# Kernel optimization log

Hardware: AMD Instinct MI355X
Metric: run time of the kernel (lower is better)

Reference implementation:

```python
import jax, jax.numpy as jnp
import numpy as np

BANDWIDTH = 1.0  # init arg `bandwidth`
N, V, C = 8, 2048, 64


def setup_inputs() -> dict:
    key = jax.random.key(0)
    k1, k2 = jax.random.split(key)
    x = jax.random.normal(k1, (N, V, C), dtype=jnp.float32)
    # nn.Parameter(torch.rand(V, V)) -> uniform[0,1)
    weight = jax.random.uniform(k2, (V, V), dtype=jnp.float32)
    return {"x": x, "weight": weight}


def _pairwise_l2(x):
    # x: (N, V, C) -> dist[n,i,j] = ||x[n,i] - x[n,j]||_2, without the O(V^2*C) blow-up
    sq = jnp.sum(x * x, axis=-1)                                  # (N, V)
    d2 = sq[:, :, None] + sq[:, None, :] - 2.0 * jnp.einsum('nic,njc->nij', x, x)
    d2 = jnp.maximum(d2, 0.0)
    # safe sqrt: subgradient 0 at 0 (matches torch.norm), avoids NaN grads on the diagonal
    safe = jnp.where(d2 > 0, d2, 1.0)
    return jnp.where(d2 > 0, jnp.sqrt(safe), 0.0)


def reference(x, weight):
    dist = _pairwise_l2(x)                                        # (N, V, V)
    adj = jnp.exp((-0.5 / (BANDWIDTH ** 2)) * dist)               # Gaussian kernel on L2 (not squared)
    adj = jnp.einsum('nij,jk->nik', adj, weight)                  # (N, V, V) @ (V, V)
    return jax.nn.softmax(adj, axis=-1)
```

## Files before the change

### kernel.cpp

```cpp
#include <hip/hip_runtime.h>
#include <hip/hip_bf16.h>
#include <hip/hip_fp16.h>
#include <math.h>

#define V 2048
#define C 64
#define NB 8
#define M_TOTAL (NB * V)

typedef __attribute__((ext_vector_type(8))) short bf16x8;
typedef __attribute__((ext_vector_type(4))) float f32x4;

static __device__ __forceinline__ unsigned short f2bf(float f) {
    __hip_bfloat16 h = __float2bfloat16(f);
    return *reinterpret_cast<unsigned short*>(&h);
}
static __device__ __forceinline__ unsigned short f2h(float f) {
    __half h = __float2half(f);
    return *reinterpret_cast<unsigned short*>(&h);
}
static __device__ __forceinline__ float h2f(unsigned short u) {
    __half h = *reinterpret_cast<__half*>(&u);
    return __half2float(h);
}

#define GLOAD_LDS16(g, l)                                                        \
    __builtin_amdgcn_global_load_lds((const __attribute__((address_space(1))) void*)(g), \
                                     (__attribute__((address_space(3))) void*)(l), 16, 0, 0)


__global__ __launch_bounds__(256) void adj_mfma(const float* __restrict__ x,
                                                unsigned short* __restrict__ adjb) {
    const int n  = blockIdx.z;
    const int i0 = blockIdx.y * 128;
    const int j0 = blockIdx.x * 128;
    const size_t nV = (size_t)n * V;

    __shared__ short Xi[128][72];
    __shared__ short Xj[128][72];
    __shared__ float Qi[128];
    __shared__ float Qj[128];

    const float* xn = x + nV * C;
    const int tid = threadIdx.x;

    for (int idx = tid; idx < 1024; idx += 256) {
        const int row = idx >> 3;
        const int c8  = (idx & 7) * 8;
        float4 ai0 = *(const float4*)(xn + (size_t)(i0 + row) * C + c8);
        float4 ai1 = *(const float4*)(xn + (size_t)(i0 + row) * C + c8 + 4);
        float4 aj0 = *(const float4*)(xn + (size_t)(j0 + row) * C + c8);
        float4 aj1 = *(const float4*)(xn + (size_t)(j0 + row) * C + c8 + 4);
        bf16x8 pi, pj;
        pi[0] = (short)f2bf(ai0.x); pi[1] = (short)f2bf(ai0.y);
        pi[2] = (short)f2bf(ai0.z); pi[3] = (short)f2bf(ai0.w);
        pi[4] = (short)f2bf(ai1.x); pi[5] = (short)f2bf(ai1.y);
        pi[6] = (short)f2bf(ai1.z); pi[7] = (short)f2bf(ai1.w);
        pj[0] = (short)f2bf(aj0.x); pj[1] = (short)f2bf(aj0.y);
        pj[2] = (short)f2bf(aj0.z); pj[3] = (short)f2bf(aj0.w);
        pj[4] = (short)f2bf(aj1.x); pj[5] = (short)f2bf(aj1.y);
        pj[6] = (short)f2bf(aj1.z); pj[7] = (short)f2bf(aj1.w);
        *(bf16x8*)&Xi[row][c8] = pi;
        *(bf16x8*)&Xj[row][c8] = pj;
    }
    __syncthreads();

    const int wid  = tid >> 6;
    const int lane = tid & 63;
    const int wr = wid >> 1, wc = wid & 1;
    const int lr = lane & 15, lq = lane >> 4;

#pragma unroll
    for (int gg = 0; gg < 2; ++gg) {
        const int g = wid * 2 + gg;
        {
            const short* xr = &Xi[g * 16 + lr][0];
            bf16x8 a0 = *(const bf16x8*)(xr + lq * 8);
            bf16x8 a1 = *(const bf16x8*)(xr + 32 + lq * 8);
            f32x4 qa = (f32x4){0.f, 0.f, 0.f, 0.f};
            qa = __builtin_amdgcn_mfma_f32_16x16x32_bf16(a0, a0, qa, 0, 0, 0);
            qa = __builtin_amdgcn_mfma_f32_16x16x32_bf16(a1, a1, qa, 0, 0, 0);
            if (lq == (lr >> 2)) Qi[g * 16 + lr] = qa[lr & 3];
        }
        {
            const short* xr = &Xj[g * 16 + lr][0];
            bf16x8 a0 = *(const bf16x8*)(xr + lq * 8);
            bf16x8 a1 = *(const bf16x8*)(xr + 32 + lq * 8);
            f32x4 qa = (f32x4){0.f, 0.f, 0.f, 0.f};
            qa = __builtin_amdgcn_mfma_f32_16x16x32_bf16(a0, a0, qa, 0, 0, 0);
            qa = __builtin_amdgcn_mfma_f32_16x16x32_bf16(a1, a1, qa, 0, 0, 0);
            if (lq == (lr >> 2)) Qj[g * 16 + lr] = qa[lr & 3];
        }
    }
    __syncthreads();

    bf16x8 a[4][2], b[4][2];
#pragma unroll
    for (int m = 0; m < 4; ++m) {
        a[m][0] = *(const bf16x8*)&Xi[wr * 64 + m * 16 + lr][lq * 8];
        a[m][1] = *(const bf16x8*)&Xi[wr * 64 + m * 16 + lr][32 + lq * 8];
    }
#pragma unroll
    for (int nn = 0; nn < 4; ++nn) {
        b[nn][0] = *(const bf16x8*)&Xj[wc * 64 + nn * 16 + lr][lq * 8];
        b[nn][1] = *(const bf16x8*)&Xj[wc * 64 + nn * 16 + lr][32 + lq * 8];
    }

#pragma unroll
    for (int m = 0; m < 4; ++m) {
#pragma unroll
        for (int nn = 0; nn < 4; ++nn) {
            f32x4 g = (f32x4){0.f, 0.f, 0.f, 0.f};
            g = __builtin_amdgcn_mfma_f32_16x16x32_bf16(a[m][0], b[nn][0], g, 0, 0, 0);
            g = __builtin_amdgcn_mfma_f32_16x16x32_bf16(a[m][1], b[nn][1], g, 0, 0, 0);
            const int col_l = wc * 64 + nn * 16 + lr;
            const float qj = Qj[col_l];
#pragma unroll
            for (int r = 0; r < 4; ++r) {
                const int row_l = wr * 64 + m * 16 + lq * 4 + r;
                float d2 = Qi[row_l] + qj - 2.0f * g[r];
                d2 = fmaxf(d2, 0.0f);
                const float e = __expf(-0.5f * sqrtf(d2));
                adjb[(nV + i0 + row_l) * V + j0 + col_l] = f2bf(e);
            }
        }
    }
}

__global__ __launch_bounds__(256) void wt_kernel(const float* __restrict__ w,
                                                 unsigned short* __restrict__ wt) {
    __shared__ float tile[64][65];
    const int r0 = blockIdx.y * 64, c0 = blockIdx.x * 64;
    const int tr = threadIdx.x >> 4;
    const int tc4 = (threadIdx.x & 15) << 2;
#pragma unroll
    for (int it = 0; it < 4; ++it) {
        const int r = tr + 16 * it;
        float4 v = *(const float4*)(w + (size_t)(r0 + r) * V + c0 + tc4);
        tile[r][tc4 + 0] = v.x; tile[r][tc4 + 1] = v.y;
        tile[r][tc4 + 2] = v.z; tile[r][tc4 + 3] = v.w;
    }
    __syncthreads();
#pragma unroll
    for (int it = 0; it < 4; ++it) {
        const int cr = tr + 16 * it;
        ushort4 o;
        o.x = f2bf(tile[tc4 + 0][cr]);
        o.y = f2bf(tile[tc4 + 1][cr]);
        o.z = f2bf(tile[tc4 + 2][cr]);
        o.w = f2bf(tile[tc4 + 3][cr]);
        *(ushort4*)(wt + (size_t)(c0 + cr) * V + r0 + tc4) = o;
    }
}

__device__ __forceinline__ void stage_region(char* smem, int regionOff,
                                             const unsigned short* gbase,
                                             int tile, int ks, int tid) {
#pragma unroll
    for (int s = 0; s < 2; ++s) {
        const int off = s * 8192 + tid * 16;
        const int row = off >> 6;
        const int pb  = off & 63;
        const int lb  = pb ^ (((row >> 1) & 3) << 4);
        const unsigned short* g = gbase + (size_t)row * V + tile * 64 + ks * 32 + (lb >> 1);
        GLOAD_LDS16(g, smem + regionOff + off);
    }
}

#define LDS_FRAG(BUF, BOFF, KS, ROW)                                             \
    (*(const bf16x8*)(smem + (BUF) * 65536 + (BOFF) + (KS) * 16384 +             \
                      (ROW) * 64 + (lqb ^ ((((ROW) >> 1) & 3) << 4))))

#define PHASE(BUF, MS, KS, LOADB, STAGE_STMT, WAITV)                             \
    {                                                                            \
        bf16x8 af[4];                                                            \
        _Pragma("unroll") for (int m = 0; m < 4; ++m) {                          \
            const int row = wr128 + ((MS) + m) * 16 + lr;                        \
            af[m] = LDS_FRAG(BUF, 0, KS, row);                                   \
        }                                                                        \
        if (LOADB) {                                                             \
            _Pragma("unroll") for (int n = 0; n < 4; ++n) {                      \
                const int row = wc64 + n * 16 + lr;                              \
                bf[n] = LDS_FRAG(BUF, 32768, KS, row);                           \
            }                                                                    \
        }                                                                        \
        STAGE_STMT;                                                              \
        if (WAITV) {                                                             \
            asm volatile("s_waitcnt vmcnt(6)" ::: "memory");                     \
            __builtin_amdgcn_sched_barrier(0);                                   \
        }                                                                        \
        __builtin_amdgcn_s_barrier();                                            \
        asm volatile("s_waitcnt lgkmcnt(0)" ::: "memory");                       \
        __builtin_amdgcn_sched_barrier(0);                                       \
        __builtin_amdgcn_s_setprio(1);                                           \
        _Pragma("unroll") for (int m = 0; m < 4; ++m)                            \
            _Pragma("unroll") for (int n = 0; n < 4; ++n)                        \
                acc[(MS) + m][n] = __builtin_amdgcn_mfma_f32_16x16x32_bf16(      \
                    af[m], bf[n], acc[(MS) + m][n], 0, 0, 0);                    \
        __builtin_amdgcn_s_setprio(0);                                           \
        __builtin_amdgcn_s_barrier();                                            \
    }

template <int FUSED>
__global__ __launch_bounds__(512, 2) void gemm_8ph(const unsigned short* __restrict__ adjb,
                                                   const unsigned short* __restrict__ wtb,
                                                   float* __restrict__ out,
                                                   unsigned short* __restrict__ expw) {
    extern __shared__ char smem[];

    const int bid = blockIdx.x;
    const int swz = (bid & 7) * 64 + (bid >> 3);
    const int by = swz >> 3;
    const int bx = swz & 7;
    const int i0 = by * 256;
    const int n0 = bx * 256;

    const int tid  = threadIdx.x;
    const int wid  = tid >> 6;
    const int lane = tid & 63;
    const int wr = wid >> 2, wc = wid & 3;
    const int wr128 = wr * 128, wc64 = wc * 64;
    const int lr = lane & 15, lq = lane >> 4;
    const int lqb = lq * 16;

    const unsigned short* gA = adjb + (size_t)i0 * V;
    const unsigned short* gB = wtb  + (size_t)n0 * V;

    f32x4 acc[8][4];
#pragma unroll
    for (int m = 0; m < 8; ++m)
#pragma unroll
        for (int n = 0; n < 4; ++n) acc[m][n] = (f32x4){0.f, 0.f, 0.f, 0.f};

    stage_region(smem, 32768,         gB, 0, 0, tid);
    stage_region(smem, 0,             gA, 0, 0, tid);
    stage_region(smem, 49152,         gB, 0, 1, tid);
    stage_region(smem, 16384,         gA, 0, 1, tid);
    stage_region(smem, 65536 + 32768, gB, 1, 0, tid);
    stage_region(smem, 65536 + 0,     gA, 1, 0, tid);
    stage_region(smem, 65536 + 49152, gB, 1, 1, tid);
    asm volatile("s_waitcnt vmcnt(6)" ::: "memory");
    __builtin_amdgcn_sched_barrier(0);
    __builtin_amdgcn_s_barrier();

    bf16x8 bf[4];

#pragma unroll 1
    for (int i = 0; i < 16; ++i) {
        const int t1b = 2 * i + 1;
        const int t2  = (2 * i + 2 < 32) ? 2 * i + 2 : 31;
        const int t3  = (2 * i + 3 < 32) ? 2 * i + 3 : 31;

        PHASE(0, 0, 0, true,  stage_region(smem, 65536 + 16384, gA, t1b, 1, tid), false)
        PHASE(0, 4, 0, false, stage_region(smem, 32768,         gB, t2,  0, tid), false)
        PHASE(0, 0, 1, true,  stage_region(smem, 0,             gA, t2,  0, tid), false)
        PHASE(0, 4, 1, false, stage_region(smem, 49152,         gB, t2,  1, tid), true)
        PHASE(1, 0, 0, true,  stage_region(smem, 16384,         gA, t2,  1, tid), false)
        PHASE(1, 4, 0, false, stage_region(smem, 65536 + 32768, gB, t3,  0, tid), false)
        PHASE(1, 0, 1, true,  stage_region(smem, 65536 + 0,     gA, t3,  0, tid), false)
        PHASE(1, 4, 1, false, stage_region(smem, 65536 + 49152, gB, t3,  1, tid), true)
    }

    if (FUSED) {
        unsigned short* ep = expw + (size_t)(i0 + wr128) * V + n0 + wc64;
#pragma unroll
        for (int m = 0; m < 8; ++m) {
#pragma unroll
            for (int r = 0; r < 4; ++r) {
                unsigned short* p = ep + (size_t)(m * 16 + lq * 4 + r) * V;
#pragma unroll
                for (int n = 0; n < 4; ++n)
                    p[n * 16 + lr] = f2h(__expf(acc[m][n][r]));
            }
        }
    } else {
        float* op = out + (size_t)(i0 + wr128) * V + n0 + wc64;
#pragma unroll
        for (int m = 0; m < 8; ++m)
#pragma unroll
            for (int n = 0; n < 4; ++n)
#pragma unroll
                for (int r = 0; r < 4; ++r)
                    op[(size_t)(m * 16 + lq * 4 + r) * V + n * 16 + lr] = acc[m][n][r];
    }
}

__global__ __launch_bounds__(256) void normalize_kernel(const unsigned short* __restrict__ expw,
                                                        float* __restrict__ out) {
    const int row  = blockIdx.x * 4 + (threadIdx.x >> 6);
    const int lane = threadIdx.x & 63;

    const unsigned short* ip = expw + (size_t)row * V;
    float* op = out + (size_t)row * V;

    float v[32];
    float sum = 0.0f;
#pragma unroll
    for (int t = 0; t < 4; ++t) {
        const int base = (t * 64 + lane) * 8;
        ushort4 u0 = *(const ushort4*)(ip + base);
        ushort4 u1 = *(const ushort4*)(ip + base + 4);
        v[t * 8 + 0] = h2f(u0.x); v[t * 8 + 1] = h2f(u0.y);
        v[t * 8 + 2] = h2f(u0.z); v[t * 8 + 3] = h2f(u0.w);
        v[t * 8 + 4] = h2f(u1.x); v[t * 8 + 5] = h2f(u1.y);
        v[t * 8 + 6] = h2f(u1.z); v[t * 8 + 7] = h2f(u1.w);
#pragma unroll
        for (int k = 0; k < 8; ++k) sum += v[t * 8 + k];
    }
#pragma unroll
    for (int o = 32; o; o >>= 1) sum += __shfl_xor(sum, o);
    const float inv = 1.0f / sum;

#pragma unroll
    for (int t = 0; t < 4; ++t) {
        const int base = (t * 64 + lane) * 8;
        float4 o0, o1;
        o0.x = v[t * 8 + 0] * inv; o0.y = v[t * 8 + 1] * inv;
        o0.z = v[t * 8 + 2] * inv; o0.w = v[t * 8 + 3] * inv;
        o1.x = v[t * 8 + 4] * inv; o1.y = v[t * 8 + 5] * inv;
        o1.z = v[t * 8 + 6] * inv; o1.w = v[t * 8 + 7] * inv;
        *(float4*)(op + base)     = o0;
        *(float4*)(op + base + 4) = o1;
    }
}

__global__ __launch_bounds__(256) void gemm_mfma(const unsigned short* __restrict__ adjb,
                                                 const unsigned short* __restrict__ wtb,
                                                 float* __restrict__ out) {
    const int bid = blockIdx.x;
    const int swz = (bid & 7) * 256 + (bid >> 3);
    const int by = swz >> 4;
    const int bx = swz & 15;
    const int i0 = by * 128;
    const int n0 = bx * 128;

    __shared__ alignas(16) unsigned short As[128 * 32];
    __shared__ alignas(16) unsigned short Bs[128 * 32];

    const int tid  = threadIdx.x;
    const int wid  = tid >> 6;
    const int lane = tid & 63;
    const int wr = wid >> 1, wc = wid & 1;
    const int lr = lane & 15, lq = lane >> 4;

    f32x4 acc[4][4];
#pragma unroll
    for (int m = 0; m < 4; ++m)
#pragma unroll
        for (int n = 0; n < 4; ++n) acc[m][n] = (f32x4){0.f, 0.f, 0.f, 0.f};

    const unsigned short* ga = adjb + (size_t)(i0 + (tid >> 2)) * V + (tid & 3) * 8;
    const unsigned short* gb = wtb  + (size_t)(n0 + (tid >> 2)) * V + (tid & 3) * 8;
    unsigned short* lA = &As[tid * 8];
    unsigned short* lB = &Bs[tid * 8];
    const size_t rowskip = (size_t)64 * V;

    for (int kt = 0; kt < 64; ++kt) {
        const int k0 = kt * 32;
        if (kt) __syncthreads();
        GLOAD_LDS16(ga + k0,           lA);
        GLOAD_LDS16(ga + rowskip + k0, lA + 256 * 8);
        GLOAD_LDS16(gb + k0,           lB);
        GLOAD_LDS16(gb + rowskip + k0, lB + 256 * 8);
        __syncthreads();

        bf16x8 a[4], b[4];
#pragma unroll
        for (int m = 0; m < 4; ++m)
            a[m] = *(const bf16x8*)&As[(wr * 64 + m * 16 + lr) * 32 + lq * 8];
#pragma unroll
        for (int n = 0; n < 4; ++n)
            b[n] = *(const bf16x8*)&Bs[(wc * 64 + n * 16 + lr) * 32 + lq * 8];
#pragma unroll
        for (int m = 0; m < 4; ++m)
#pragma unroll
            for (int n = 0; n < 4; ++n)
                acc[m][n] = __builtin_amdgcn_mfma_f32_16x16x32_bf16(a[m], b[n], acc[m][n], 0, 0, 0);
    }

    float* outp = out + (size_t)(i0 + wr * 64) * V + n0 + wc * 64;
#pragma unroll
    for (int m = 0; m < 4; ++m) {
        const int r0 = m * 16 + lq * 4;
#pragma unroll
        for (int n = 0; n < 4; ++n) {
            const int cc = n * 16 + lr;
#pragma unroll
            for (int r = 0; r < 4; ++r)
                outp[(size_t)(r0 + r) * V + cc] = acc[m][n][r];
        }
    }
}


__global__ __launch_bounds__(256) void adj_kernel(const float* __restrict__ x,
                                                  float* __restrict__ adj) {
    const int n  = blockIdx.z;
    const int i0 = blockIdx.y * 64;
    const int j0 = blockIdx.x * 64;

    __shared__ float Xi[64][65];
    __shared__ float Xj[64][65];

    const float* xn = x + (size_t)n * V * C;
    const int tid = threadIdx.x;
    const int lr = tid >> 4;
    const int lc = (tid & 15) << 2;
#pragma unroll
    for (int it = 0; it < 4; ++it) {
        const int r = lr + it * 16;
        float4 vi = *(const float4*)(xn + (size_t)(i0 + r) * C + lc);
        float4 vj = *(const float4*)(xn + (size_t)(j0 + r) * C + lc);
        Xi[r][lc + 0] = vi.x; Xi[r][lc + 1] = vi.y; Xi[r][lc + 2] = vi.z; Xi[r][lc + 3] = vi.w;
        Xj[r][lc + 0] = vj.x; Xj[r][lc + 1] = vj.y; Xj[r][lc + 2] = vj.z; Xj[r][lc + 3] = vj.w;
    }
    __syncthreads();

    const int ti = (tid >> 4) << 2;
    const int tj = (tid & 15) << 2;

    float acc[4][4] = {};
#pragma unroll 4
    for (int c = 0; c < C; ++c) {
        float ai[4], bj[4];
#pragma unroll
        for (int a = 0; a < 4; ++a) ai[a] = Xi[ti + a][c];
#pragma unroll
        for (int b = 0; b < 4; ++b) bj[b] = Xj[tj + b][c];
#pragma unroll
        for (int a = 0; a < 4; ++a)
#pragma unroll
            for (int b = 0; b < 4; ++b) {
                const float d = ai[a] - bj[b];
                acc[a][b] = fmaf(d, d, acc[a][b]);
            }
    }

    float* outb = adj + ((size_t)n * V + i0) * V + j0;
#pragma unroll
    for (int a = 0; a < 4; ++a) {
        float4 o0;
        o0.x = expf(-0.5f * sqrtf(acc[a][0]));
        o0.y = expf(-0.5f * sqrtf(acc[a][1]));
        o0.z = expf(-0.5f * sqrtf(acc[a][2]));
        o0.w = expf(-0.5f * sqrtf(acc[a][3]));
        *(float4*)(outb + (size_t)(ti + a) * V + tj) = o0;
    }
}

__global__ __launch_bounds__(256) void gemm_inplace(float* __restrict__ adjout,
                                                    const float* __restrict__ w) {
    const int n  = blockIdx.y;
    const int i0 = blockIdx.x * 8;

    __shared__ float rows[8][V];

    float* base = adjout + ((size_t)n * V + i0) * V;
    const int tid = threadIdx.x;

    for (int t = tid; t < (8 * V) / 4; t += 256) {
        const int r = t >> 9;
        const int c = (t & 511) << 2;
        float4 v = *(const float4*)(base + (size_t)r * V + c);
        rows[r][c + 0] = v.x; rows[r][c + 1] = v.y; rows[r][c + 2] = v.z; rows[r][c + 3] = v.w;
    }
    __syncthreads();

    float acc[8][8] = {};
    const int k0 = tid << 3;
    const float* wp = w + k0;

    for (int j = 0; j < V; ++j) {
        float a[8];
#pragma unroll
        for (int r = 0; r < 8; ++r) a[r] = rows[r][j];
        const float* wr = wp + (size_t)j * V;
        const float4 w0 = *(const float4*)(wr);
        const float4 w1 = *(const float4*)(wr + 4);
        const float wv[8] = {w0.x, w0.y, w0.z, w0.w, w1.x, w1.y, w1.z, w1.w};
#pragma unroll
        for (int r = 0; r < 8; ++r)
#pragma unroll
            for (int c = 0; c < 8; ++c)
                acc[r][c] = fmaf(a[r], wv[c], acc[r][c]);
    }

#pragma unroll
    for (int r = 0; r < 8; ++r) {
        float4 o0, o1;
        o0.x = acc[r][0]; o0.y = acc[r][1]; o0.z = acc[r][2]; o0.w = acc[r][3];
        o1.x = acc[r][4]; o1.y = acc[r][5]; o1.z = acc[r][6]; o1.w = acc[r][7];
        *(float4*)(base + (size_t)r * V + k0)     = o0;
        *(float4*)(base + (size_t)r * V + k0 + 4) = o1;
    }
}

__global__ __launch_bounds__(256) void softmax_kernel(float* __restrict__ out) {
    const int row  = blockIdx.x * 4 + (threadIdx.x >> 6);
    const int lane = threadIdx.x & 63;
    float* p = out + (size_t)row * V;

    float4 v[8];
#pragma unroll
    for (int s = 0; s < 8; ++s)
        v[s] = *(const float4*)(p + (size_t)(s * 64 + lane) * 4);

    float m = -INFINITY;
#pragma unroll
    for (int s = 0; s < 8; ++s)
        m = fmaxf(m, fmaxf(fmaxf(v[s].x, v[s].y), fmaxf(v[s].z, v[s].w)));
#pragma unroll
    for (int o = 32; o; o >>= 1) m = fmaxf(m, __shfl_xor(m, o));

    float sum = 0.0f;
#pragma unroll
    for (int s = 0; s < 8; ++s) {
        v[s].x = expf(v[s].x - m);
        v[s].y = expf(v[s].y - m);
        v[s].z = expf(v[s].z - m);
        v[s].w = expf(v[s].w - m);
        sum += (v[s].x + v[s].y) + (v[s].z + v[s].w);
    }
#pragma unroll
    for (int o = 32; o; o >>= 1) sum += __shfl_xor(sum, o);

    const float inv = 1.0f / sum;
#pragma unroll
    for (int s = 0; s < 8; ++s) {
        float4 o4;
        o4.x = v[s].x * inv; o4.y = v[s].y * inv;
        o4.z = v[s].z * inv; o4.w = v[s].w * inv;
        *(float4*)(p + (size_t)(s * 64 + lane) * 4) = o4;
    }
}

extern "C" void kernel_launch(void* const* d_in, const int* in_sizes, int n_in,
                              void* d_out, int out_size, void* d_ws, size_t ws_size,
                              hipStream_t stream) {
    const float* x = (const float*)d_in[0];
    const float* w = (const float*)d_in[1];
    float* out = (float*)d_out;

    const size_t adj_elems = (size_t)M_TOTAL * V;
    const size_t wt_elems  = (size_t)V * V;
    const size_t need      = (adj_elems + wt_elems) * 2;
    const size_t exp_off   = need;
    const size_t need_big  = exp_off + adj_elems * 2;

    if (ws_size >= need) {
        unsigned short* adjb = (unsigned short*)d_ws;
        unsigned short* wtb  = adjb + adj_elems;

        adj_mfma<<<dim3(V / 128, V / 128, NB), 256, 0, stream>>>(x, adjb);
        wt_kernel<<<dim3(V / 64, V / 64), 256, 0, stream>>>(w, wtb);

        if (ws_size >= need_big) {
            unsigned short* expw = (unsigned short*)((char*)d_ws + exp_off);
            hipError_t ok = hipFuncSetAttribute(
                reinterpret_cast<const void*>(&gemm_8ph<1>),
                hipFuncAttributeMaxDynamicSharedMemorySize, 131072);
            if (ok == hipSuccess) {
                gemm_8ph<1><<<512, 512, 131072, stream>>>(adjb, wtb, out, expw);
                normalize_kernel<<<M_TOTAL / 4, 256, 0, stream>>>(expw, out);
                return;
            }
        }
        hipError_t ok = hipFuncSetAttribute(
            reinterpret_cast<const void*>(&gemm_8ph<0>),
            hipFuncAttributeMaxDynamicSharedMemorySize, 131072);
        if (ok == hipSuccess) {
            gemm_8ph<0><<<512, 512, 131072, stream>>>(adjb, wtb, out, nullptr);
        } else {
            gemm_mfma<<<2048, 256, 0, stream>>>(adjb, wtb, out);
        }
        softmax_kernel<<<(NB * V) / 4, 256, 0, stream>>>(out);
    } else {
        dim3 g1(V / 64, V / 64, NB);
        adj_kernel<<<g1, 256, 0, stream>>>(x, out);
        dim3 g2(V / 8, NB);
        gemm_inplace<<<g2, 256, 0, stream>>>(out, w);
        softmax_kernel<<<(NB * V) / 4, 256, 0, stream>>>(out);
    }
}
```

Baseline: 188.8 us.

## Switch main GEMM to 32x32x16 MFMA tiles and use nontemporal normalize stores

Reworks the 8-phase GEMM inner loop to use the 32x32x16 bf16 MFMA instruction instead of 16x16x32. The LDS fragment addressing, register accumulator layout and epilogue row mapping change to match the new output layout. Larger MFMA tiles mean fewer instructions and fewer LDS fragment reads per unit of work, though each fragment load covers a different lane pattern that may change bank-conflict behaviour. Separately, the softmax normalize kernel now writes its output with nontemporal stores to avoid polluting cache with streaming data.

Result: slower. 217.1 us (+15.0%).

```diff
diff --git a/kernel.cpp b/kernel.cpp
--- a/kernel.cpp
+++ b/kernel.cpp
@@ -10,6 +10,7 @@
 
 typedef __attribute__((ext_vector_type(8))) short bf16x8;
 typedef __attribute__((ext_vector_type(4))) float f32x4;
+typedef __attribute__((ext_vector_type(16))) float f32x16;
 
 static __device__ __forceinline__ unsigned short f2bf(float f) {
     __hip_bfloat16 h = __float2bfloat16(f);
@@ -167,22 +168,21 @@
     }
 }
 
-#define LDS_FRAG(BUF, BOFF, KS, ROW)                                             \
+#define LDS_FRAG32(BUF, BOFF, KS, KB, ROW)                                       \
     (*(const bf16x8*)(smem + (BUF) * 65536 + (BOFF) + (KS) * 16384 +             \
-                      (ROW) * 64 + (lqb ^ ((((ROW) >> 1) & 3) << 4))))
-
-#define PHASE(BUF, MS, KS, LOADB, STAGE_STMT, WAITV)                             \
+                      (ROW) * 64 + ((((KB) * 32) + lkb) ^ ((((ROW) >> 1) & 3) << 4))))
+
+#define PHASE32(BUF, MH, KS, LOADB, STAGE_STMT, WAITV)                           \
     {                                                                            \
-        bf16x8 af[4];                                                            \
-        _Pragma("unroll") for (int m = 0; m < 4; ++m) {                          \
-            const int row = wr128 + ((MS) + m) * 16 + lr;                        \
-            af[m] = LDS_FRAG(BUF, 0, KS, row);                                   \
-        }                                                                        \
+        bf16x8 af00 = LDS_FRAG32(BUF, 0, KS, 0, wr128 + ((MH) * 2 + 0) * 32 + l31); \
+        bf16x8 af01 = LDS_FRAG32(BUF, 0, KS, 1, wr128 + ((MH) * 2 + 0) * 32 + l31); \
+        bf16x8 af10 = LDS_FRAG32(BUF, 0, KS, 0, wr128 + ((MH) * 2 + 1) * 32 + l31); \
+        bf16x8 af11 = LDS_FRAG32(BUF, 0, KS, 1, wr128 + ((MH) * 2 + 1) * 32 + l31); \
         if (LOADB) {                                                             \
-            _Pragma("unroll") for (int n = 0; n < 4; ++n) {                      \
-                const int row = wc64 + n * 16 + lr;                              \
-                bf[n] = LDS_FRAG(BUF, 32768, KS, row);                           \
-            }                                                                    \
+            bf[0][0] = LDS_FRAG32(BUF, 32768, KS, 0, wc64 + l31);                \
+            bf[0][1] = LDS_FRAG32(BUF, 32768, KS, 1, wc64 + l31);                \
+            bf[1][0] = LDS_FRAG32(BUF, 32768, KS, 0, wc64 + 32 + l31);           \
+            bf[1][1] = LDS_FRAG32(BUF, 32768, KS, 1, wc64 + 32 + l31);           \
         }                                                                        \
         STAGE_STMT;                                                              \
         if (WAITV) {                                                             \
@@ -193,10 +193,14 @@
         asm volatile("s_waitcnt lgkmcnt(0)" ::: "memory");                       \
         __builtin_amdgcn_sched_barrier(0);                                       \
         __builtin_amdgcn_s_setprio(1);                                           \
-        _Pragma("unroll") for (int m = 0; m < 4; ++m)                            \
-            _Pragma("unroll") for (int n = 0; n < 4; ++n)                        \
-                acc[(MS) + m][n] = __builtin_amdgcn_mfma_f32_16x16x32_bf16(      \
-                    af[m], bf[n], acc[(MS) + m][n], 0, 0, 0);                    \
+        acc32[(MH) * 2 + 0][0] = __builtin_amdgcn_mfma_f32_32x32x16_bf16(af00, bf[0][0], acc32[(MH) * 2 + 0][0], 0, 0, 0); \
+        acc32[(MH) * 2 + 0][0] = __builtin_amdgcn_mfma_f32_32x32x16_bf16(af01, bf[0][1], acc32[(MH) * 2 + 0][0], 0, 0, 0); \
+        acc32[(MH) * 2 + 0][1] = __builtin_amdgcn_mfma_f32_32x32x16_bf16(af00, bf[1][0], acc32[(MH) * 2 + 0][1], 0, 0, 0); \
+        acc32[(MH) * 2 + 0][1] = __builtin_amdgcn_mfma_f32_32x32x16_bf16(af01, bf[1][1], acc32[(MH) * 2 + 0][1], 0, 0, 0); \
+        acc32[(MH) * 2 + 1][0] = __builtin_amdgcn_mfma_f32_32x32x16_bf16(af10, bf[0][0], acc32[(MH) * 2 + 1][0], 0, 0, 0); \
+        acc32[(MH) * 2 + 1][0] = __builtin_amdgcn_mfma_f32_32x32x16_bf16(af11, bf[0][1], acc32[(MH) * 2 + 1][0], 0, 0, 0); \
+        acc32[(MH) * 2 + 1][1] = __builtin_amdgcn_mfma_f32_32x32x16_bf16(af10, bf[1][0], acc32[(MH) * 2 + 1][1], 0, 0, 0); \
+        acc32[(MH) * 2 + 1][1] = __builtin_amdgcn_mfma_f32_32x32x16_bf16(af11, bf[1][1], acc32[(MH) * 2 + 1][1], 0, 0, 0); \
         __builtin_amdgcn_s_setprio(0);                                           \
         __builtin_amdgcn_s_barrier();                                            \
     }
@@ -220,17 +224,19 @@
     const int lane = tid & 63;
     const int wr = wid >> 2, wc = wid & 3;
     const int wr128 = wr * 128, wc64 = wc * 64;
-    const int lr = lane & 15, lq = lane >> 4;
-    const int lqb = lq * 16;
+    const int l31 = lane & 31, l5 = lane >> 5;
+    const int lkb = l5 * 16;
 
     const unsigned short* gA = adjb + (size_t)i0 * V;
     const unsigned short* gB = wtb  + (size_t)n0 * V;
 
-    f32x4 acc[8][4];
-#pragma unroll
-    for (int m = 0; m < 8; ++m)
-#pragma unroll
-        for (int n = 0; n < 4; ++n) acc[m][n] = (f32x4){0.f, 0.f, 0.f, 0.f};
+    f32x16 acc32[4][2];
+#pragma unroll
+    for (int m = 0; m < 4; ++m)
+#pragma unroll
+        for (int n = 0; n < 2; ++n)
+#pragma unroll
+            for (int g = 0; g < 16; ++g) acc32[m][n][g] = 0.f;
 
     stage_region(smem, 32768,         gB, 0, 0, tid);
     stage_region(smem, 0,             gA, 0, 0, tid);
@@ -243,7 +249,7 @@
     __builtin_amdgcn_sched_barrier(0);
     __builtin_amdgcn_s_barrier();
 
-    bf16x8 bf[4];
+    bf16x8 bf[2][2];
 
 #pragma unroll 1
     for (int i = 0; i < 16; ++i) {
@@ -251,37 +257,38 @@
         const int t2  = (2 * i + 2 < 32) ? 2 * i + 2 : 31;
         const int t3  = (2 * i + 3 < 32) ? 2 * i + 3 : 31;
 
-        PHASE(0, 0, 0, true,  stage_region(smem, 65536 + 16384, gA, t1b, 1, tid), false)
-        PHASE(0, 4, 0, false, stage_region(smem, 32768,         gB, t2,  0, tid), false)
-        PHASE(0, 0, 1, true,  stage_region(smem, 0,             gA, t2,  0, tid), false)
-        PHASE(0, 4, 1, false, stage_region(smem, 49152,         gB, t2,  1, tid), true)
-        PHASE(1, 0, 0, true,  stage_region(smem, 16384,         gA, t2,  1, tid), false)
-        PHASE(1, 4, 0, false, stage_region(smem, 65536 + 32768, gB, t3,  0, tid), false)
-        PHASE(1, 0, 1, true,  stage_region(smem, 65536 + 0,     gA, t3,  0, tid), false)
-        PHASE(1, 4, 1, false, stage_region(smem, 65536 + 49152, gB, t3,  1, tid), true)
+        PHASE32(0, 0, 0, true,  stage_region(smem, 65536 + 16384, gA, t1b, 1, tid), false)
+        PHASE32(0, 1, 0, false, stage_region(smem, 32768,         gB, t2,  0, tid), false)
+        PHASE32(0, 0, 1, true,  stage_region(smem, 0,             gA, t2,  0, tid), false)
+        PHASE32(0, 1, 1, false, stage_region(smem, 49152,         gB, t2,  1, tid), true)
+        PHASE32(1, 0, 0, true,  stage_region(smem, 16384,         gA, t2,  1, tid), false)
+        PHASE32(1, 1, 0, false, stage_region(smem, 65536 + 32768, gB, t3,  0, tid), false)
+        PHASE32(1, 0, 1, true,  stage_region(smem, 65536 + 0,     gA, t3,  0, tid), false)
+        PHASE32(1, 1, 1, false, stage_region(smem, 65536 + 49152, gB, t3,  1, tid), true)
     }
 
     if (FUSED) {
         unsigned short* ep = expw + (size_t)(i0 + wr128) * V + n0 + wc64;
 #pragma unroll
-        for (int m = 0; m < 8; ++m) {
-#pragma unroll
-            for (int r = 0; r < 4; ++r) {
-                unsigned short* p = ep + (size_t)(m * 16 + lq * 4 + r) * V;
-#pragma unroll
-                for (int n = 0; n < 4; ++n)
-                    p[n * 16 + lr] = f2h(__expf(acc[m][n][r]));
+        for (int m = 0; m < 4; ++m)
+#pragma unroll
+            for (int g = 0; g < 16; ++g) {
+                const int row = m * 32 + (g & 3) + 8 * (g >> 2) + 4 * l5;
+#pragma unroll
+                for (int n = 0; n < 2; ++n)
+                    ep[(size_t)row * V + n * 32 + l31] = f2h(__expf(acc32[m][n][g]));
             }
-        }
     } else {
         float* op = out + (size_t)(i0 + wr128) * V + n0 + wc64;
 #pragma unroll
-        for (int m = 0; m < 8; ++m)
-#pragma unroll
-            for (int n = 0; n < 4; ++n)
-#pragma unroll
-                for (int r = 0; r < 4; ++r)
-                    op[(size_t)(m * 16 + lq * 4 + r) * V + n * 16 + lr] = acc[m][n][r];
+        for (int m = 0; m < 4; ++m)
+#pragma unroll
+            for (int g = 0; g < 16; ++g) {
+                const int row = m * 32 + (g & 3) + 8 * (g >> 2) + 4 * l5;
+#pragma unroll
+                for (int n = 0; n < 2; ++n)
+                    op[(size_t)row * V + n * 32 + l31] = acc32[m][n][g];
+            }
     }
 }
 
@@ -314,13 +321,13 @@
 #pragma unroll
     for (int t = 0; t < 4; ++t) {
         const int base = (t * 64 + lane) * 8;
-        float4 o0, o1;
-        o0.x = v[t * 8 + 0] * inv; o0.y = v[t * 8 + 1] * inv;
-        o0.z = v[t * 8 + 2] * inv; o0.w = v[t * 8 + 3] * inv;
-        o1.x = v[t * 8 + 4] * inv; o1.y = v[t * 8 + 5] * inv;
-        o1.z = v[t * 8 + 6] * inv; o1.w = v[t * 8 + 7] * inv;
-        *(float4*)(op + base)     = o0;
-        *(float4*)(op + base + 4) = o1;
+        f32x4 o0, o1;
+        o0[0] = v[t * 8 + 0] * inv; o0[1] = v[t * 8 + 1] * inv;
+        o0[2] = v[t * 8 + 2] * inv; o0[3] = v[t * 8 + 3] * inv;
+        o1[0] = v[t * 8 + 4] * inv; o1[1] = v[t * 8 + 5] * inv;
+        o1[2] = v[t * 8 + 6] * inv; o1[3] = v[t * 8 + 7] * inv;
+        __builtin_nontemporal_store(o0, (f32x4*)(op + base));
+        __builtin_nontemporal_store(o1, (f32x4*)(op + base + 4));
     }
 }
 
```
